# Kernel tuning notes

Measured on AMD Instinct MI355X. Metric: run time of the kernel, lower is better.

The kernel has to match this reference:

```python
import jax, jax.numpy as jnp
import numpy as np

N_NODES = 50000
N_EDGES = 1600000
IN_DIM, HID_DIM, OUT_DIM, HEADS = 128, 128, 64, 8
NEG_SLOPE = 0.2
BN_EPS = 1e-5


def setup_inputs() -> dict:
    key = jax.random.key(0)
    ks = jax.random.split(key, 12)
    hpc = HID_DIM // HEADS  # per-head channels of layer 1
    return {
        "x": jax.random.normal(ks[0], (N_NODES, IN_DIM), jnp.float32),
        "edge_index": jax.random.randint(ks[1], (2, N_EDGES), 0, N_NODES, jnp.int64),
        "W1": jax.random.normal(ks[2], (IN_DIM, HEADS * hpc), jnp.float32) * 0.05,
        "a1_src": jax.random.normal(ks[3], (HEADS, hpc), jnp.float32) * 0.1,
        "a1_dst": jax.random.normal(ks[4], (HEADS, hpc), jnp.float32) * 0.1,
        "b1": jnp.zeros((HEADS * hpc,), jnp.float32),
        "bn_gamma": jnp.ones((HID_DIM,), jnp.float32),
        "bn_beta": jnp.zeros((HID_DIM,), jnp.float32),
        "W2": jax.random.normal(ks[5], (HID_DIM, OUT_DIM), jnp.float32) * 0.05,
        "a2_src": jax.random.normal(ks[6], (1, OUT_DIM), jnp.float32) * 0.1,
        "a2_dst": jax.random.normal(ks[7], (1, OUT_DIM), jnp.float32) * 0.1,
        "b2": jnp.zeros((OUT_DIM,), jnp.float32),
    }


def _gat_conv(x, src, dst, W, a_src, a_dst, bias, heads, n_nodes):
    # x: [N, Fin]; src/dst: [E'] (self-loops already appended)
    hpc = W.shape[1] // heads
    h = (x @ W).reshape(n_nodes, heads, hpc)                 # [N,H,C]
    alpha_s = jnp.einsum("nhc,hc->nh", h, a_src)             # [N,H]
    alpha_d = jnp.einsum("nhc,hc->nh", h, a_dst)
    e = alpha_s[src] + alpha_d[dst]                          # [E',H]
    e = jax.nn.leaky_relu(e, NEG_SLOPE)
    # segment softmax over destination neighborhoods
    m = jax.ops.segment_max(e, dst, num_segments=n_nodes)    # [N,H]
    m = jnp.where(jnp.isfinite(m), m, 0.0)
    ee = jnp.exp(e - m[dst])
    denom = jax.ops.segment_sum(ee, dst, num_segments=n_nodes)
    alpha = ee / (denom[dst] + 1e-16)                        # [E',H]
    msg = h[src] * alpha[:, :, None]                         # [E',H,C]
    out = jax.ops.segment_sum(msg, dst, num_segments=n_nodes)  # [N,H,C]
    return out.reshape(n_nodes, heads * hpc) + bias


def _batch_norm(x, gamma, beta):
    mu = jnp.mean(x, axis=0)
    var = jnp.var(x, axis=0)
    return gamma * (x - mu) * jax.lax.rsqrt(var + BN_EPS) + beta


def reference(x, edge_index, W1, a1_src, a1_dst, b1, bn_gamma, bn_beta, W2, a2_src, a2_dst, b2):
    n = x.shape[0]
    loops = jnp.arange(n, dtype=edge_index.dtype)
    src = jnp.concatenate([edge_index[0], loops])            # PyG add_self_loops
    dst = jnp.concatenate([edge_index[1], loops])
    h = _gat_conv(x, src, dst, W1, a1_src, a1_dst, b1, HEADS, n)
    h = _batch_norm(h, bn_gamma, bn_beta)
    h = jax.nn.elu(h)
    # dropout: identity at inference
    out = _gat_conv(h, src, dst, W2, a2_src, a2_dst, b2, 1, n)
    return out
```

## Files before the change

kernel.cpp:

```cpp
#include <hip/hip_runtime.h>
#include <hip/hip_bf16.h>

#define N_NODES 50000
#define N_EDGES 1600000
#define HEADS 8
#define NBK 196
#define NBLK 196
#define EPB 8192

typedef unsigned short u16;
typedef unsigned char u8;
typedef unsigned int u32;
typedef __attribute__((ext_vector_type(8))) short bf16x8;
typedef __attribute__((ext_vector_type(4))) float f32x4;

__device__ __forceinline__ float bf2f(u16 u) {
  union { u32 i; float f; } v; v.i = ((u32)u) << 16; return v.f;
}
__device__ __forceinline__ float bflo(u32 p) {
  union { u32 i; float f; } v; v.i = p << 16; return v.f;
}
__device__ __forceinline__ float bfhi(u32 p) {
  union { u32 i; float f; } v; v.i = p & 0xffff0000u; return v.f;
}
__device__ __forceinline__ u16 f2bf(float f) {
  union { float f; u32 i; } v; v.f = f;
  u32 r = v.i + 0x7fff + ((v.i >> 16) & 1);
  return (u16)(r >> 16);
}
__device__ __forceinline__ u32 pack2(float a, float b) {
  return (u32)f2bf(a) | ((u32)f2bf(b) << 16);
}
__device__ __forceinline__ int rfl(int x) { return __builtin_amdgcn_readfirstlane(x); }

__global__ void k_detect(const u16* __restrict__ x, const u32* __restrict__ ei,
                         int* __restrict__ flags) {
  __shared__ int cbig, cnz;
  if (threadIdx.x == 0) { cbig = 0; cnz = 0; }
  __syncthreads();
  int lb = 0, ln = 0;
  for (int i = threadIdx.x; i < 4096; i += 256) {
    int ex = (x[i] >> 7) & 0xff;
    lb += (ex >= 140);
    if (i < 2048) ln += (ei[2 * i + 1] != 0);
  }
  atomicAdd(&cbig, lb); atomicAdd(&cnz, ln);
  __syncthreads();
  if (threadIdx.x == 0) {
    flags[0] = (cbig > 16) ? 1 : 0;
    flags[1] = (cnz == 0) ? 1 : 0;
  }
}

__global__ void k_convsmall(const void* a1s, const void* a1d, const void* b1,
                            const void* gam, const void* bet, const void* a2s,
                            const void* a2d, const void* b2, const void* W1,
                            const void* W2, float* __restrict__ smallf,
                            u16* __restrict__ w1t, u16* __restrict__ w2t,
                            const int* __restrict__ flags) {
  int i = blockIdx.x * 256 + threadIdx.x;
  if (i >= 25408) return;
  bool f32 = flags[0] != 0;
  auto ld = [&](const void* p, int off) -> float {
    return f32 ? ((const float*)p)[off] : bf2f(((const u16*)p)[off]);
  };
  if (i >= 17216) {
    int j = i - 17216, n = j >> 7, k = j & 127;
    w2t[j] = f2bf(ld(W2, k * 64 + n));
  } else if (i >= 832) {
    int j = i - 832, n = j >> 7, k = j & 127;
    w1t[j] = f2bf(ld(W1, k * 128 + n));
  } else {
    const void* src; int off;
    if (i >= 768)      { src = b2;  off = i - 768; }
    else if (i >= 704) { src = a2d; off = i - 704; }
    else if (i >= 640) { src = a2s; off = i - 640; }
    else if (i >= 512) { src = bet; off = i - 512; }
    else if (i >= 384) { src = gam; off = i - 384; }
    else if (i >= 256) { src = b1;  off = i - 256; }
    else if (i >= 128) { src = a1d; off = i - 128; }
    else               { src = a1s; off = i; }
    smallf[i] = ld(src, off);
  }
}

__global__ __launch_bounds__(256) void k_hist(const int* __restrict__ ei,
                                              int* __restrict__ H,
                                              int* __restrict__ totals,
                                              const int* __restrict__ flags) {
  __shared__ int hist[NBK];
  int t = threadIdx.x, blk = blockIdx.x;
  for (int i = t; i < NBK; i += 256) hist[i] = 0;
  __syncthreads();
  bool i64 = flags[1] != 0;
  int base = blk * EPB;
  for (int k = 0; k < 32; k++) {
    int e = base + k * 256 + t;
    if (e < N_EDGES) {
      int d = i64 ? ei[2 * (N_EDGES + e)] : ei[N_EDGES + e];
      atomicAdd(&hist[d >> 8], 1);
    }
  }
  __syncthreads();
  for (int i = t; i < NBK; i += 256) {
    H[i * NBLK + blk] = hist[i];
    atomicAdd(&totals[i], hist[i]);
  }
}

__global__ void k_scan_tot(const int* __restrict__ totals, int* __restrict__ bucketBase) {
  __shared__ int tmp[256];
  int t = threadIdx.x;
  int v = (t < NBK) ? totals[t] : 0;
  tmp[t] = v; __syncthreads();
  for (int o = 1; o < 256; o <<= 1) {
    int x = (t >= o) ? tmp[t - o] : 0; __syncthreads();
    tmp[t] += x; __syncthreads();
  }
  if (t < NBK) bucketBase[t] = tmp[t] - v;
  if (t == NBK - 1) bucketBase[NBK] = tmp[t];
}

__global__ void k_scan_blk(const int* __restrict__ H, const int* __restrict__ bucketBase,
                           int* __restrict__ P) {
  __shared__ int tmp[256];
  int t = threadIdx.x, b = blockIdx.x;
  int v = (t < NBLK) ? H[b * NBLK + t] : 0;
  tmp[t] = v; __syncthreads();
  for (int o = 1; o < 256; o <<= 1) {
    int x = (t >= o) ? tmp[t - o] : 0; __syncthreads();
    tmp[t] += x; __syncthreads();
  }
  if (t < NBLK) P[b * NBLK + t] = bucketBase[b] + tmp[t] - v;
}

__global__ __launch_bounds__(256) void k_bucket(const int* __restrict__ ei,
                                                const int* __restrict__ P,
                                                u32* __restrict__ buf,
                                                const int* __restrict__ flags) {
  __shared__ u32 sv[EPB];
  __shared__ u16 rank[EPB];
  __shared__ u8  sk8[EPB];
  __shared__ int cnt[NBK], scn[NBK], tmp[256];
  int t = threadIdx.x, blk = blockIdx.x;
  int base = blk * EPB;
  int nE = N_EDGES - base; if (nE > EPB) nE = EPB;
  for (int i = t; i < NBK; i += 256) cnt[i] = 0;
  __syncthreads();
  bool i64 = flags[1] != 0;
  for (int k = 0; k < EPB / 256; k++) {
    int li = k * 256 + t, e = base + li;
    if (li < nE) {
      int d = i64 ? ei[2 * (N_EDGES + e)] : ei[N_EDGES + e];
      rank[li] = (u16)atomicAdd(&cnt[d >> 8], 1);
    }
  }
  __syncthreads();
  int v = (t < NBK) ? cnt[t] : 0;
  tmp[t] = v; __syncthreads();
  for (int o = 1; o < 256; o <<= 1) {
    int x = (t >= o) ? tmp[t - o] : 0; __syncthreads();
    tmp[t] += x; __syncthreads();
  }
  if (t < NBK) scn[t] = tmp[t] - v;
  __syncthreads();
  for (int k = 0; k < EPB / 256; k++) {
    int li = k * 256 + t, e = base + li;
    if (li < nE) {
      int s = i64 ? ei[2 * e] : ei[e];
      int d = i64 ? ei[2 * (N_EDGES + e)] : ei[N_EDGES + e];
      int key = d >> 8;
      int pos = scn[key] + rank[li];
      sv[pos] = ((u32)(d & 255) << 16) | (u32)s;
      sk8[pos] = (u8)key;
    }
  }
  __syncthreads();
  for (int i = t; i < nE; i += 256) {
    int b = sk8[i];
    buf[P[b * NBLK + blk] + (i - scn[b])] = sv[i];
  }
}

__global__ __launch_bounds__(256) void k_csr(const u32* __restrict__ buf,
                                             const int* __restrict__ bucketBase,
                                             int* __restrict__ row_start,
                                             int* __restrict__ deg,
                                             int* __restrict__ csr, int N) {
  __shared__ int cnt[256], scn[256], cur[256];
  int b = blockIdx.x, t = threadIdx.x;
  int lo = bucketBase[b], hi = bucketBase[b + 1];
  cnt[t] = 0; __syncthreads();
  for (int e = lo + t; e < hi; e += 256) atomicAdd(&cnt[(buf[e] >> 16) & 255], 1);
  __syncthreads();
  int v = cnt[t];
  scn[t] = v; __syncthreads();
  for (int o = 1; o < 256; o <<= 1) {
    int x = (t >= o) ? scn[t - o] : 0; __syncthreads();
    scn[t] += x; __syncthreads();
  }
  int excl = scn[t] - v;
  int node = b * 256 + t;
  if (node < N) { row_start[node] = lo + excl; deg[node] = v; }
  cur[t] = lo + excl;
  __syncthreads();
  for (int e = lo + t; e < hi; e += 256) {
    u32 p = buf[e];
    int pos = atomicAdd(&cur[(p >> 16) & 255], 1);
    csr[pos] = p & 0xffff;
  }
}

template <int NCOLS, bool EPI, bool ALPHA1, bool AFLAG>
__global__ __launch_bounds__(256) void k_gemm_mfma(const void* __restrict__ A,
                                                   const u16* __restrict__ BT,
                                                   const float* __restrict__ scale,
                                                   const float* __restrict__ shift,
                                                   const float* __restrict__ va,
                                                   const float* __restrict__ vb,
                                                   float* __restrict__ as_out,
                                                   float* __restrict__ ad_out,
                                                   u16* __restrict__ C, int M,
                                                   const int* __restrict__ flags) {
  constexpr int KP = 136;
  constexpr int NT = NCOLS / 16;
  __shared__ u16 As[64 * KP];
  __shared__ u16 Bs[NCOLS * KP];
  int t = threadIdx.x;
  int row0 = blockIdx.x * 64;
  bool af32 = AFLAG ? (flags[0] != 0) : false;

  for (int i = t; i < NCOLS * 16; i += 256) {
    int n = i >> 4, q = i & 15;
    *(uint4*)&Bs[n * KP + q * 8] = ((const uint4*)BT)[n * 16 + q];
  }
  for (int i = t; i < 64 * 32; i += 256) {
    int r = i >> 5, c4 = i & 31;
    int row = row0 + r;
    uint2 pk = make_uint2(0u, 0u);
    if (row < M) {
      if (EPI) {
        uint2 p = ((const uint2*)A)[(size_t)row * 32 + c4];
        int c = c4 * 4;
        float v0 = bflo(p.x), v1 = bfhi(p.x), v2 = bflo(p.y), v3 = bfhi(p.y);
        v0 = fmaf(v0, scale[c],     shift[c]);     v0 = v0 > 0.f ? v0 : __expf(v0) - 1.f;
        v1 = fmaf(v1, scale[c + 1], shift[c + 1]); v1 = v1 > 0.f ? v1 : __expf(v1) - 1.f;
        v2 = fmaf(v2, scale[c + 2], shift[c + 2]); v2 = v2 > 0.f ? v2 : __expf(v2) - 1.f;
        v3 = fmaf(v3, scale[c + 3], shift[c + 3]); v3 = v3 > 0.f ? v3 : __expf(v3) - 1.f;
        pk.x = pack2(v0, v1); pk.y = pack2(v2, v3);
      } else if (af32) {
        float4 v = ((const float4*)A)[(size_t)row * 32 + c4];
        pk.x = pack2(v.x, v.y); pk.y = pack2(v.z, v.w);
      } else {
        pk = ((const uint2*)A)[(size_t)row * 32 + c4];
      }
    }
    *(uint2*)&As[r * KP + c4 * 4] = pk;
  }
  __syncthreads();

  int lane = t & 63, w = t >> 6;
  int m = lane & 15, quad = lane >> 4;
  f32x4 acc[NT];
#pragma unroll
  for (int nt = 0; nt < NT; nt++) acc[nt] = (f32x4)(0.f);
  const u16* aBase = &As[(w * 16 + m) * KP + quad * 8];
  const u16* bBase = &Bs[m * KP + quad * 8];
#pragma unroll
  for (int ks = 0; ks < 4; ks++) {
    bf16x8 af = *(const bf16x8*)(aBase + ks * 32);
#pragma unroll
    for (int nt = 0; nt < NT; nt++) {
      bf16x8 bf = *(const bf16x8*)(bBase + nt * 16 * KP + ks * 32);
      acc[nt] = __builtin_amdgcn_mfma_f32_16x16x32_bf16(af, bf, acc[nt], 0, 0, 0);
    }
  }
  int orow0 = row0 + w * 16 + quad * 4;
#pragma unroll
  for (int nt = 0; nt < NT; nt++) {
#pragma unroll
    for (int r = 0; r < 4; r++) {
      int row = orow0 + r;
      if (row < M) C[(size_t)row * NCOLS + nt * 16 + m] = f2bf(acc[nt][r]);
    }
  }
  if (ALPHA1) {
    float pav[NT], pbv[NT];
#pragma unroll
    for (int nt = 0; nt < NT; nt++) { pav[nt] = va[nt * 16 + m]; pbv[nt] = vb[nt * 16 + m]; }
#pragma unroll
    for (int r = 0; r < 4; r++) {
      int row = orow0 + r;
#pragma unroll
      for (int nt = 0; nt < NT; nt++) {
        float vs = acc[nt][r] * pav[nt];
        float vd = acc[nt][r] * pbv[nt];
        vs += __shfl_xor(vs, 1); vd += __shfl_xor(vd, 1);
        vs += __shfl_xor(vs, 2); vd += __shfl_xor(vd, 2);
        vs += __shfl_xor(vs, 4); vd += __shfl_xor(vd, 4);
        vs += __shfl_xor(vs, 8); vd += __shfl_xor(vd, 8);
        if (row < M && m == 0) { as_out[row * 8 + nt] = vs; ad_out[row * 8 + nt] = vd; }
      }
    }
  }
  if (EPI) {
    float pav[NT], pbv[NT];
#pragma unroll
    for (int nt = 0; nt < NT; nt++) { pav[nt] = va[nt * 16 + m]; pbv[nt] = vb[nt * 16 + m]; }
#pragma unroll
    for (int r = 0; r < 4; r++) {
      float vs = 0.f, vd = 0.f;
#pragma unroll
      for (int nt = 0; nt < NT; nt++) {
        vs = fmaf(acc[nt][r], pav[nt], vs);
        vd = fmaf(acc[nt][r], pbv[nt], vd);
      }
      vs += __shfl_xor(vs, 1); vd += __shfl_xor(vd, 1);
      vs += __shfl_xor(vs, 2); vd += __shfl_xor(vd, 2);
      vs += __shfl_xor(vs, 4); vd += __shfl_xor(vd, 4);
      vs += __shfl_xor(vs, 8); vd += __shfl_xor(vd, 8);
      int row = orow0 + r;
      if (row < M && m == 0) { as_out[row] = vs; ad_out[row] = vd; }
    }
  }
}

__global__ __launch_bounds__(256) void k_agg1(const u16* __restrict__ h1b,
                                              const float* __restrict__ as_,
                                              const float* __restrict__ ad_,
                                              const int* __restrict__ csr,
                                              const int* __restrict__ row_start,
                                              const int* __restrict__ deg,
                                              const float* __restrict__ b1,
                                              u16* __restrict__ out,
                                              float* __restrict__ bnrep, int N) {
  __shared__ float lsum[128], lsq[128];
  int t = threadIdx.x;
  if (t < 128) { lsum[t] = 0.f; lsq[t] = 0.f; }
  __syncthreads();
  int node = blockIdx.x * 4 + (t >> 6);
  int l = t & 63;
  int head = l >> 3, sub = l & 7;
  int eh = l >> 5, c2 = l & 31;
  int hch = c2 >> 2;
  if (node < N) {
    int node_u = rfl(node);
    int st = rfl(row_start[node_u]);
    int cnt = rfl(deg[node_u]);
    const int* cp = csr + st;
    const uint2* h2p = (const uint2*)h1b;
    float ad = ad_[(node_u << 3) | head];
    float sp = 0.f, a0 = 0.f, a1 = 0.f, a2 = 0.f, a3 = 0.f;
    int j = 0;
    for (; j + 8 <= cnt; j += 8) {
      int ssub = cp[j + sub];
      float e = as_[(ssub << 3) | head] + ad;
      e = fmaxf(e, 0.2f * e);
      float p = __expf(e);
      sp += p;
#pragma unroll
      for (int k = 0; k < 4; k++) {
        int se = cp[j + 2 * k], so = cp[j + 2 * k + 1];
        int sk = eh ? so : se;
        float pk = __shfl(p, (hch << 3) | (2 * k + eh));
        uint2 hv = h2p[(size_t)sk * 32 + c2];
        a0 = fmaf(pk, bflo(hv.x), a0); a1 = fmaf(pk, bfhi(hv.x), a1);
        a2 = fmaf(pk, bflo(hv.y), a2); a3 = fmaf(pk, bfhi(hv.y), a3);
      }
    }
    for (; j <= cnt; j++) {
      int s0 = (j < cnt) ? rfl(cp[j]) : node_u;
      float e = as_[(s0 << 3) | head] + ad;
      e = fmaxf(e, 0.2f * e);
      float p = __expf(e);
      if (sub == 0) sp += p;
      float pk = __shfl(p, hch << 3);
      if (eh == 0) {
        uint2 hv = h2p[(size_t)s0 * 32 + c2];
        a0 = fmaf(pk, bflo(hv.x), a0); a1 = fmaf(pk, bfhi(hv.x), a1);
        a2 = fmaf(pk, bflo(hv.y), a2); a3 = fmaf(pk, bfhi(hv.y), a3);
      }
    }
    sp += __shfl_xor(sp, 1);
    sp += __shfl_xor(sp, 2);
    sp += __shfl_xor(sp, 4);
    float inv = 1.f / (__shfl(sp, hch << 3) + 1e-16f);
    a0 += __shfl_xor(a0, 32); a1 += __shfl_xor(a1, 32);
    a2 += __shfl_xor(a2, 32); a3 += __shfl_xor(a3, 32);
    if (eh == 0) {
      int c0 = c2 * 4;
      float r0 = fmaf(a0, inv, b1[c0]);
      float r1 = fmaf(a1, inv, b1[c0 + 1]);
      float r2 = fmaf(a2, inv, b1[c0 + 2]);
      float r3 = fmaf(a3, inv, b1[c0 + 3]);
      ((uint2*)out)[(size_t)node_u * 32 + c2] = make_uint2(pack2(r0, r1), pack2(r2, r3));
      atomicAdd(&lsum[c0], r0);     atomicAdd(&lsq[c0], r0 * r0);
      atomicAdd(&lsum[c0 + 1], r1); atomicAdd(&lsq[c0 + 1], r1 * r1);
      atomicAdd(&lsum[c0 + 2], r2); atomicAdd(&lsq[c0 + 2], r2 * r2);
      atomicAdd(&lsum[c0 + 3], r3); atomicAdd(&lsq[c0 + 3], r3 * r3);
    }
  }
  __syncthreads();
  if (t < 128) {
    int rep = (blockIdx.x & 31) * 256;
    atomicAdd(&bnrep[rep + t], lsum[t]);
    atomicAdd(&bnrep[rep + 128 + t], lsq[t]);
  }
}

__global__ void k_bnfin(const float* __restrict__ bnrep,
                        const float* __restrict__ gamma, const float* __restrict__ beta,
                        float* __restrict__ scale, float* __restrict__ shift, int N) {
  int t = threadIdx.x;
  if (t >= 128) return;
  float s = 0.f, q = 0.f;
  for (int r = 0; r < 32; r++) {
    s += bnrep[r * 256 + t];
    q += bnrep[r * 256 + 128 + t];
  }
  float mu = s / (float)N;
  float var = fmaxf(q / (float)N - mu * mu, 0.f);
  float sc = gamma[t] * rsqrtf(var + 1e-5f);
  scale[t] = sc;
  shift[t] = beta[t] - mu * sc;
}

__global__ __launch_bounds__(256) void k_agg2(const u16* __restrict__ h2b,
                                              const float* __restrict__ as_,
                                              const float* __restrict__ ad_,
                                              const int* __restrict__ csr,
                                              const int* __restrict__ row_start,
                                              const int* __restrict__ deg,
                                              const float* __restrict__ b2,
                                              void* __restrict__ out,
                                              const int* __restrict__ flags, int N) {
  int node = blockIdx.x * 4 + (threadIdx.x >> 6);
  if (node >= N) return;
  int l = threadIdx.x & 63;
  int sub = l & 7;
  int e4 = l >> 4, c4 = l & 15;
  int node_u = rfl(node);
  int st = rfl(row_start[node_u]);
  int cnt = rfl(deg[node_u]);
  const int* cp = csr + st;
  const uint2* h2p = (const uint2*)h2b;
  float ad = ad_[node_u];
  float sp = 0.f, a0 = 0.f, a1 = 0.f, a2 = 0.f, a3 = 0.f;
  int j = 0;
  for (; j + 8 <= cnt; j += 8) {
    int ssub = cp[j + sub];
    float e = as_[ssub] + ad;
    e = fmaxf(e, 0.2f * e);
    float p = __expf(e);
    if (l < 8) sp += p;
#pragma unroll
    for (int pass = 0; pass < 2; pass++) {
      int sa = cp[j + 4 * pass], sb = cp[j + 4 * pass + 1];
      int sc = cp[j + 4 * pass + 2], sd = cp[j + 4 * pass + 3];
      int sk = (e4 == 0) ? sa : (e4 == 1) ? sb : (e4 == 2) ? sc : sd;
      float pk = __shfl(p, 4 * pass + e4);
      uint2 hv = h2p[(size_t)sk * 16 + c4];
      a0 = fmaf(pk, bflo(hv.x), a0); a1 = fmaf(pk, bfhi(hv.x), a1);
      a2 = fmaf(pk, bflo(hv.y), a2); a3 = fmaf(pk, bfhi(hv.y), a3);
    }
  }
  for (; j <= cnt; j++) {
    int s0 = (j < cnt) ? rfl(cp[j]) : node_u;
    float e = as_[s0] + ad;
    e = fmaxf(e, 0.2f * e);
    float p = __expf(e);
    if (l == 0) sp += p;
    float pk = __shfl(p, 0);
    if (e4 == 0) {
      uint2 hv = h2p[(size_t)s0 * 16 + c4];
      a0 = fmaf(pk, bflo(hv.x), a0); a1 = fmaf(pk, bfhi(hv.x), a1);
      a2 = fmaf(pk, bflo(hv.y), a2); a3 = fmaf(pk, bfhi(hv.y), a3);
    }
  }
  sp += __shfl_xor(sp, 1);
  sp += __shfl_xor(sp, 2);
  sp += __shfl_xor(sp, 4);
  float inv = 1.f / (__shfl(sp, 0) + 1e-16f);
  a0 += __shfl_xor(a0, 16); a1 += __shfl_xor(a1, 16);
  a2 += __shfl_xor(a2, 16); a3 += __shfl_xor(a3, 16);
  a0 += __shfl_xor(a0, 32); a1 += __shfl_xor(a1, 32);
  a2 += __shfl_xor(a2, 32); a3 += __shfl_xor(a3, 32);
  if (e4 == 0) {
    int c0 = c4 * 4;
    float r0 = fmaf(a0, inv, b2[c0]);
    float r1 = fmaf(a1, inv, b2[c0 + 1]);
    float r2 = fmaf(a2, inv, b2[c0 + 2]);
    float r3 = fmaf(a3, inv, b2[c0 + 3]);
    if (flags[0]) {
      ((float4*)out)[(size_t)node_u * 16 + c4] = make_float4(r0, r1, r2, r3);
    } else {
      ((uint2*)out)[(size_t)node_u * 16 + c4] = make_uint2(pack2(r0, r1), pack2(r2, r3));
    }
  }
}

extern "C" void kernel_launch(void* const* d_in, const int* in_sizes, int n_in,
                              void* d_out, int out_size, void* d_ws, size_t ws_size,
                              hipStream_t stream) {
  const void* x   = d_in[0];
  const int*  ei  = (const int*)d_in[1];
  const void* W1  = d_in[2];
  const void* a1s = d_in[3];
  const void* a1d = d_in[4];
  const void* b1  = d_in[5];
  const void* gam = d_in[6];
  const void* bet = d_in[7];
  const void* W2  = d_in[8];
  const void* a2s = d_in[9];
  const void* a2d = d_in[10];
  const void* b2  = d_in[11];

  char* ws = (char*)d_ws;
  size_t off = 0;
  auto alloc = [&](size_t bytes) -> void* {
    void* p = ws + off;
    off += (bytes + 255) & ~(size_t)255;
    return p;
  };
  int* flags = (int*)alloc(256);
  char* zreg = (char*)alloc(1024 + 32 * 256 * 4);
  int* totals = (int*)zreg;
  float* bnrep = (float*)(zreg + 1024);
  int* H  = (int*)alloc((size_t)NBK * NBLK * 4);
  int* P  = (int*)alloc((size_t)NBK * NBLK * 4);
  int* bucketBase = (int*)alloc(1024);
  u32* ebuf = (u32*)alloc((size_t)N_EDGES * 4);
  int* csr = (int*)alloc((size_t)N_EDGES * 4);
  int* row_start = (int*)alloc((size_t)N_NODES * 4);
  int* deg = (int*)alloc((size_t)N_NODES * 4);
  float* smallf = (float*)alloc(832 * 4);
  float* a1sf = smallf;        float* a1df = smallf + 128;
  float* b1f  = smallf + 256;  float* gamf = smallf + 384;
  float* betf = smallf + 512;  float* a2sf = smallf + 640;
  float* a2df = smallf + 704;  float* b2f  = smallf + 768;
  u16* w1t = (u16*)alloc(16384 * 2);
  u16* w2t = (u16*)alloc(8192 * 2);
  u16* h1b  = (u16*)alloc((size_t)N_NODES * 128 * 2);
  u16* h1ob = (u16*)alloc((size_t)N_NODES * 128 * 2);
  u16* h2b  = (u16*)alloc((size_t)N_NODES * 64 * 2);
  float* al1s = (float*)alloc((size_t)N_NODES * 8 * 4);
  float* al1d = (float*)alloc((size_t)N_NODES * 8 * 4);
  float* scale = (float*)alloc(512);
  float* shift = (float*)alloc(512);
  float* al2s = (float*)alloc((size_t)N_NODES * 4);
  float* al2d = (float*)alloc((size_t)N_NODES * 4);
  if (off > ws_size) return;

  hipMemsetAsync(zreg, 0, 1024 + 32 * 256 * 4, stream);
  k_detect<<<1, 256, 0, stream>>>((const u16*)x, (const u32*)ei, flags);
  k_convsmall<<<100, 256, 0, stream>>>(a1s, a1d, b1, gam, bet, a2s, a2d, b2, W1, W2,
                                       smallf, w1t, w2t, flags);

  k_hist<<<NBLK, 256, 0, stream>>>(ei, H, totals, flags);
  k_scan_tot<<<1, 256, 0, stream>>>(totals, bucketBase);
  k_scan_blk<<<NBK, 256, 0, stream>>>(H, bucketBase, P);
  k_bucket<<<NBLK, 256, 0, stream>>>(ei, P, ebuf, flags);
  k_csr<<<NBK, 256, 0, stream>>>(ebuf, bucketBase, row_start, deg, csr, N_NODES);

  k_gemm_mfma<128, false, true, true><<<(N_NODES + 63) / 64, 256, 0, stream>>>(
      x, w1t, nullptr, nullptr, a1sf, a1df, al1s, al1d, h1b, N_NODES, flags);
  k_agg1<<<(N_NODES + 3) / 4, 256, 0, stream>>>(h1b, al1s, al1d, csr, row_start, deg,
                                                b1f, h1ob, bnrep, N_NODES);
  k_bnfin<<<1, 128, 0, stream>>>(bnrep, gamf, betf, scale, shift, N_NODES);

  k_gemm_mfma<64, true, false, false><<<(N_NODES + 63) / 64, 256, 0, stream>>>(
      h1ob, w2t, scale, shift, a2sf, a2df, al2s, al2d, h2b, N_NODES, flags);
  k_agg2<<<(N_NODES + 3) / 4, 256, 0, stream>>>(h2b, al2s, al2d, csr, row_start, deg,
                                                b2f, d_out, flags, N_NODES);
}
```

Baseline: 370.0 us.

## Fold scan and BN-finalize kernels into consumers; move BN stats to separate pass

```diff
diff --git a/kernel.cpp b/kernel.cpp
--- a/kernel.cpp
+++ b/kernel.cpp
@@ -108,30 +108,24 @@
   }
 }
 
-__global__ void k_scan_tot(const int* __restrict__ totals, int* __restrict__ bucketBase) {
-  __shared__ int tmp[256];
-  int t = threadIdx.x;
-  int v = (t < NBK) ? totals[t] : 0;
-  tmp[t] = v; __syncthreads();
+__global__ void k_scan_blk(const int* __restrict__ H, const int* __restrict__ totals,
+                           int* __restrict__ P) {
+  __shared__ int tb[256], tmp[256];
+  int t = threadIdx.x, b = blockIdx.x;
+  int v0 = (t < NBK) ? totals[t] : 0;
+  tb[t] = v0; __syncthreads();
   for (int o = 1; o < 256; o <<= 1) {
-    int x = (t >= o) ? tmp[t - o] : 0; __syncthreads();
-    tmp[t] += x; __syncthreads();
-  }
-  if (t < NBK) bucketBase[t] = tmp[t] - v;
-  if (t == NBK - 1) bucketBase[NBK] = tmp[t];
-}
-
-__global__ void k_scan_blk(const int* __restrict__ H, const int* __restrict__ bucketBase,
-                           int* __restrict__ P) {
-  __shared__ int tmp[256];
-  int t = threadIdx.x, b = blockIdx.x;
+    int x = (t >= o) ? tb[t - o] : 0; __syncthreads();
+    tb[t] += x; __syncthreads();
+  }
+  int base = (b == 0) ? 0 : tb[b - 1];
   int v = (t < NBLK) ? H[b * NBLK + t] : 0;
   tmp[t] = v; __syncthreads();
   for (int o = 1; o < 256; o <<= 1) {
     int x = (t >= o) ? tmp[t - o] : 0; __syncthreads();
     tmp[t] += x; __syncthreads();
   }
-  if (t < NBLK) P[b * NBLK + t] = bucketBase[b] + tmp[t] - v;
+  if (t < NBLK) P[b * NBLK + t] = base + tmp[t] - v;
 }
 
 __global__ __launch_bounds__(256) void k_bucket(const int* __restrict__ ei,
@@ -183,13 +177,20 @@
 }
 
 __global__ __launch_bounds__(256) void k_csr(const u32* __restrict__ buf,
-                                             const int* __restrict__ bucketBase,
+                                             const int* __restrict__ totals,
                                              int* __restrict__ row_start,
                                              int* __restrict__ deg,
                                              int* __restrict__ csr, int N) {
-  __shared__ int cnt[256], scn[256], cur[256];
+  __shared__ int tb[256], cnt[256], scn[256], cur[256];
   int b = blockIdx.x, t = threadIdx.x;
-  int lo = bucketBase[b], hi = bucketBase[b + 1];
+  int v0 = (t < NBK) ? totals[t] : 0;
+  tb[t] = v0; __syncthreads();
+  for (int o = 1; o < 256; o <<= 1) {
+    int x = (t >= o) ? tb[t - o] : 0; __syncthreads();
+    tb[t] += x; __syncthreads();
+  }
+  int lo = (b == 0) ? 0 : tb[b - 1];
+  int hi = tb[b];
   cnt[t] = 0; __syncthreads();
   for (int e = lo + t; e < hi; e += 256) atomicAdd(&cnt[(buf[e] >> 16) & 255], 1);
   __syncthreads();
@@ -214,8 +215,10 @@
 template <int NCOLS, bool EPI, bool ALPHA1, bool AFLAG>
 __global__ __launch_bounds__(256) void k_gemm_mfma(const void* __restrict__ A,
                                                    const u16* __restrict__ BT,
-                                                   const float* __restrict__ scale,
-                                                   const float* __restrict__ shift,
+                                                   const float* __restrict__ bnsum,
+                                                   const float* __restrict__ bnsq,
+                                                   const float* __restrict__ gamma,
+                                                   const float* __restrict__ beta,
                                                    const float* __restrict__ va,
                                                    const float* __restrict__ vb,
                                                    float* __restrict__ as_out,
@@ -226,9 +229,20 @@
   constexpr int NT = NCOLS / 16;
   __shared__ u16 As[64 * KP];
   __shared__ u16 Bs[NCOLS * KP];
+  __shared__ float sSc[128], sSh[128];
   int t = threadIdx.x;
   int row0 = blockIdx.x * 64;
   bool af32 = AFLAG ? (flags[0] != 0) : false;
+
+  if (EPI) {
+    if (t < 128) {
+      float mu = bnsum[t] * (1.f / (float)N_NODES);
+      float var = fmaxf(bnsq[t] * (1.f / (float)N_NODES) - mu * mu, 0.f);
+      float sc = gamma[t] * rsqrtf(var + 1e-5f);
+      sSc[t] = sc; sSh[t] = beta[t] - mu * sc;
+    }
+    __syncthreads();
+  }
 
   for (int i = t; i < NCOLS * 16; i += 256) {
     int n = i >> 4, q = i & 15;
@@ -243,10 +257,10 @@
         uint2 p = ((const uint2*)A)[(size_t)row * 32 + c4];
         int c = c4 * 4;
         float v0 = bflo(p.x), v1 = bfhi(p.x), v2 = bflo(p.y), v3 = bfhi(p.y);
-        v0 = fmaf(v0, scale[c],     shift[c]);     v0 = v0 > 0.f ? v0 : __expf(v0) - 1.f;
-        v1 = fmaf(v1, scale[c + 1], shift[c + 1]); v1 = v1 > 0.f ? v1 : __expf(v1) - 1.f;
-        v2 = fmaf(v2, scale[c + 2], shift[c + 2]); v2 = v2 > 0.f ? v2 : __expf(v2) - 1.f;
-        v3 = fmaf(v3, scale[c + 3], shift[c + 3]); v3 = v3 > 0.f ? v3 : __expf(v3) - 1.f;
+        v0 = fmaf(v0, sSc[c],     sSh[c]);     v0 = v0 > 0.f ? v0 : __expf(v0) - 1.f;
+        v1 = fmaf(v1, sSc[c + 1], sSh[c + 1]); v1 = v1 > 0.f ? v1 : __expf(v1) - 1.f;
+        v2 = fmaf(v2, sSc[c + 2], sSh[c + 2]); v2 = v2 > 0.f ? v2 : __expf(v2) - 1.f;
+        v3 = fmaf(v3, sSc[c + 3], sSh[c + 3]); v3 = v3 > 0.f ? v3 : __expf(v3) - 1.f;
         pk.x = pack2(v0, v1); pk.y = pack2(v2, v3);
       } else if (af32) {
         float4 v = ((const float4*)A)[(size_t)row * 32 + c4];
@@ -332,97 +346,84 @@
                                               const int* __restrict__ row_start,
                                               const int* __restrict__ deg,
                                               const float* __restrict__ b1,
-                                              u16* __restrict__ out,
-                                              float* __restrict__ bnrep, int N) {
-  __shared__ float lsum[128], lsq[128];
-  int t = threadIdx.x;
-  if (t < 128) { lsum[t] = 0.f; lsq[t] = 0.f; }
-  __syncthreads();
-  int node = blockIdx.x * 4 + (t >> 6);
-  int l = t & 63;
+                                              u16* __restrict__ out, int N) {
+  int node = blockIdx.x * 4 + (threadIdx.x >> 6);
+  if (node >= N) return;
+  int l = threadIdx.x & 63;
   int head = l >> 3, sub = l & 7;
   int eh = l >> 5, c2 = l & 31;
   int hch = c2 >> 2;
-  if (node < N) {
-    int node_u = rfl(node);
-    int st = rfl(row_start[node_u]);
-    int cnt = rfl(deg[node_u]);
-    const int* cp = csr + st;
-    const uint2* h2p = (const uint2*)h1b;
-    float ad = ad_[(node_u << 3) | head];
-    float sp = 0.f, a0 = 0.f, a1 = 0.f, a2 = 0.f, a3 = 0.f;
-    int j = 0;
-    for (; j + 8 <= cnt; j += 8) {
-      int ssub = cp[j + sub];
-      float e = as_[(ssub << 3) | head] + ad;
-      e = fmaxf(e, 0.2f * e);
-      float p = __expf(e);
-      sp += p;
-#pragma unroll
-      for (int k = 0; k < 4; k++) {
-        int se = cp[j + 2 * k], so = cp[j + 2 * k + 1];
-        int sk = eh ? so : se;
-        float pk = __shfl(p, (hch << 3) | (2 * k + eh));
-        uint2 hv = h2p[(size_t)sk * 32 + c2];
-        a0 = fmaf(pk, bflo(hv.x), a0); a1 = fmaf(pk, bfhi(hv.x), a1);
-        a2 = fmaf(pk, bflo(hv.y), a2); a3 = fmaf(pk, bfhi(hv.y), a3);
-      }
-    }
-    for (; j <= cnt; j++) {
-      int s0 = (j < cnt) ? rfl(cp[j]) : node_u;
-      float e = as_[(s0 << 3) | head] + ad;
-      e = fmaxf(e, 0.2f * e);
-      float p = __expf(e);
-      if (sub == 0) sp += p;
-      float pk = __shfl(p, hch << 3);
-      if (eh == 0) {
-        uint2 hv = h2p[(size_t)s0 * 32 + c2];
-        a0 = fmaf(pk, bflo(hv.x), a0); a1 = fmaf(pk, bfhi(hv.x), a1);
-        a2 = fmaf(pk, bflo(hv.y), a2); a3 = fmaf(pk, bfhi(hv.y), a3);
-      }
-    }
-    sp += __shfl_xor(sp, 1);
-    sp += __shfl_xor(sp, 2);
-    sp += __shfl_xor(sp, 4);
-    float inv = 1.f / (__shfl(sp, hch << 3) + 1e-16f);
-    a0 += __shfl_xor(a0, 32); a1 += __shfl_xor(a1, 32);
-    a2 += __shfl_xor(a2, 32); a3 += __shfl_xor(a3, 32);
+  int node_u = rfl(node);
+  int st = rfl(row_start[node_u]);
+  int cnt = rfl(deg[node_u]);
+  const int* cp = csr + st;
+  const uint2* h2p = (const uint2*)h1b;
+  float ad = ad_[(node_u << 3) | head];
+  float sp = 0.f, a0 = 0.f, a1 = 0.f, a2 = 0.f, a3 = 0.f;
+  int j = 0;
+  for (; j + 8 <= cnt; j += 8) {
+    int ssub = cp[j + sub];
+    float e = as_[(ssub << 3) | head] + ad;
+    e = fmaxf(e, 0.2f * e);
+    float p = __expf(e);
+    sp += p;
+#pragma unroll
+    for (int k = 0; k < 4; k++) {
+      int se = cp[j + 2 * k], so = cp[j + 2 * k + 1];
+      int sk = eh ? so : se;
+      float pk = __shfl(p, (hch << 3) | (2 * k + eh));
+      uint2 hv = h2p[(size_t)sk * 32 + c2];
+      a0 = fmaf(pk, bflo(hv.x), a0); a1 = fmaf(pk, bfhi(hv.x), a1);
+      a2 = fmaf(pk, bflo(hv.y), a2); a3 = fmaf(pk, bfhi(hv.y), a3);
+    }
+  }
+  for (; j <= cnt; j++) {
+    int s0 = (j < cnt) ? rfl(cp[j]) : node_u;
+    float e = as_[(s0 << 3) | head] + ad;
+    e = fmaxf(e, 0.2f * e);
+    float p = __expf(e);
+    if (sub == 0) sp += p;
+    float pk = __shfl(p, hch << 3);
     if (eh == 0) {
-      int c0 = c2 * 4;
-      float r0 = fmaf(a0, inv, b1[c0]);
-      float r1 = fmaf(a1, inv, b1[c0 + 1]);
-      float r2 = fmaf(a2, inv, b1[c0 + 2]);
-      float r3 = fmaf(a3, inv, b1[c0 + 3]);
-      ((uint2*)out)[(size_t)node_u * 32 + c2] = make_uint2(pack2(r0, r1), pack2(r2, r3));
-      atomicAdd(&lsum[c0], r0);     atomicAdd(&lsq[c0], r0 * r0);
-      atomicAdd(&lsum[c0 + 1], r1); atomicAdd(&lsq[c0 + 1], r1 * r1);
-      atomicAdd(&lsum[c0 + 2], r2); atomicAdd(&lsq[c0 + 2], r2 * r2);
-      atomicAdd(&lsum[c0 + 3], r3); atomicAdd(&lsq[c0 + 3], r3 * r3);
-    }
-  }
-  __syncthreads();
+      uint2 hv = h2p[(size_t)s0 * 32 + c2];
+      a0 = fmaf(pk, bflo(hv.x), a0); a1 = fmaf(pk, bfhi(hv.x), a1);
+      a2 = fmaf(pk, bflo(hv.y), a2); a3 = fmaf(pk, bfhi(hv.y), a3);
+    }
+  }
+  sp += __shfl_xor(sp, 1);
+  sp += __shfl_xor(sp, 2);
+  sp += __shfl_xor(sp, 4);
+  float inv = 1.f / (__shfl(sp, hch << 3) + 1e-16f);
+  a0 += __shfl_xor(a0, 32); a1 += __shfl_xor(a1, 32);
+  a2 += __shfl_xor(a2, 32); a3 += __shfl_xor(a3, 32);
+  if (eh == 0) {
+    int c0 = c2 * 4;
+    float r0 = fmaf(a0, inv, b1[c0]);
+    float r1 = fmaf(a1, inv, b1[c0 + 1]);
+    float r2 = fmaf(a2, inv, b1[c0 + 2]);
+    float r3 = fmaf(a3, inv, b1[c0 + 3]);
+    ((uint2*)out)[(size_t)node_u * 32 + c2] = make_uint2(pack2(r0, r1), pack2(r2, r3));
+  }
+}
+
+__global__ void k_bnstat(const u16* __restrict__ h, float* __restrict__ gsum,
+                         float* __restrict__ gsq, int N) {
+  __shared__ float ts[256], tq[256];
+  int t = threadIdx.x, col = t & 127, rr = t >> 7;
+  int row0 = blockIdx.x * 128;
+  float s = 0.f, q = 0.f;
+  for (int r = rr; r < 128; r += 2) {
+    int row = row0 + r;
+    if (row < N) {
+      float v = bf2f(h[((size_t)row << 7) + col]);
+      s += v; q = fmaf(v, v, q);
+    }
+  }
+  ts[t] = s; tq[t] = q; __syncthreads();
   if (t < 128) {
-    int rep = (blockIdx.x & 31) * 256;
-    atomicAdd(&bnrep[rep + t], lsum[t]);
-    atomicAdd(&bnrep[rep + 128 + t], lsq[t]);
-  }
-}
-
-__global__ void k_bnfin(const float* __restrict__ bnrep,
-                        const float* __restrict__ gamma, const float* __restrict__ beta,
-                        float* __restrict__ scale, float* __restrict__ shift, int N) {
-  int t = threadIdx.x;
-  if (t >= 128) return;
-  float s = 0.f, q = 0.f;
-  for (int r = 0; r < 32; r++) {
-    s += bnrep[r * 256 + t];
-    q += bnrep[r * 256 + 128 + t];
-  }
-  float mu = s / (float)N;
-  float var = fmaxf(q / (float)N - mu * mu, 0.f);
-  float sc = gamma[t] * rsqrtf(var + 1e-5f);
-  scale[t] = sc;
-  shift[t] = beta[t] - mu * sc;
+    atomicAdd(&gsum[t], ts[t] + ts[t + 128]);
+    atomicAdd(&gsq[t], tq[t] + tq[t + 128]);
+  }
 }
 
 __global__ __launch_bounds__(256) void k_agg2(const u16* __restrict__ h2b,
@@ -523,12 +524,12 @@
     return p;
   };
   int* flags = (int*)alloc(256);
-  char* zreg = (char*)alloc(1024 + 32 * 256 * 4);
+  char* zreg = (char*)alloc(2048);
   int* totals = (int*)zreg;
-  float* bnrep = (float*)(zreg + 1024);
+  float* gsum = (float*)(zreg + 1024);
+  float* gsq  = gsum + 128;
   int* H  = (int*)alloc((size_t)NBK * NBLK * 4);
   int* P  = (int*)alloc((size_t)NBK * NBLK * 4);
-  int* bucketBase = (int*)alloc(1024);
   u32* ebuf = (u32*)alloc((size_t)N_EDGES * 4);
   int* csr = (int*)alloc((size_t)N_EDGES * 4);
   int* row_start = (int*)alloc((size_t)N_NODES * 4);
@@ -545,31 +546,30 @@
   u16* h2b  = (u16*)alloc((size_t)N_NODES * 64 * 2);
   float* al1s = (float*)alloc((size_t)N_NODES * 8 * 4);
   float* al1d = (float*)alloc((size_t)N_NODES * 8 * 4);
-  float* scale = (float*)alloc(512);
-  float* shift = (float*)alloc(512);
   float* al2s = (float*)alloc((size_t)N_NODES * 4);
   float* al2d = (float*)alloc((size_t)N_NODES * 4);
   if (off > ws_size) return;
 
-  hipMemsetAsync(zreg, 0, 1024 + 32 * 256 * 4, stream);
+  hipMemsetAsync(zreg, 0, 2048, stream);
   k_detect<<<1, 256, 0, stream>>>((const u16*)x, (const u32*)ei, flags);
   k_convsmall<<<100, 256, 0, stream>>>(a1s, a1d, b1, gam, bet, a2s, a2d, b2, W1, W2,
                                        smallf, w1t, w2t, flags);
 
   k_hist<<<NBLK, 256, 0, stream>>>(ei, H, totals, flags);
-  k_scan_tot<<<1, 256, 0, stream>>>(totals, bucketBase);
-  k_scan_blk<<<NBK, 256, 0, stream>>>(H, bucketBase, P);
+  k_scan_blk<<<NBK, 256, 0, stream>>>(H, totals, P);
   k_bucket<<<NBLK, 256, 0, stream>>>(ei, P, ebuf, flags);
-  k_csr<<<NBK, 256, 0, stream>>>(ebuf, bucketBase, row_start, deg, csr, N_NODES);
+  k_csr<<<NBK, 256, 0, stream>>>(ebuf, totals, row_start, deg, csr, N_NODES);
 
   k_gemm_mfma<128, false, true, true><<<(N_NODES + 63) / 64, 256, 0, stream>>>(
-      x, w1t, nullptr, nullptr, a1sf, a1df, al1s, al1d, h1b, N_NODES, flags);
+      x, w1t, nullptr, nullptr, nullptr, nullptr, a1sf, a1df, al1s, al1d,
+      h1b, N_NODES, flags);
   k_agg1<<<(N_NODES + 3) / 4, 256, 0, stream>>>(h1b, al1s, al1d, csr, row_start, deg,
-                                                b1f, h1ob, bnrep, N_NODES);
-  k_bnfin<<<1, 128, 0, stream>>>(bnrep, gamf, betf, scale, shift, N_NODES);
+                                                b1f, h1ob, N_NODES);
+  k_bnstat<<<(N_NODES + 127) / 128, 256, 0, stream>>>(h1ob, gsum, gsq, N_NODES);
 
   k_gemm_mfma<64, true, false, false><<<(N_NODES + 63) / 64, 256, 0, stream>>>(
-      h1ob, w2t, scale, shift, a2sf, a2df, al2s, al2d, h2b, N_NODES, flags);
+      h1ob, w2t, gsum, gsq, gamf, betf, a2sf, a2df, al2s, al2d,
+      h2b, N_NODES, flags);
   k_agg2<<<(N_NODES + 3) / 4, 256, 0, stream>>>(h2b, al2s, al2d, csr, row_start, deg,
                                                 b2f, d_out, flags, N_NODES);
 }
```

Measured after the change: 357.7 us. -3.3%, faster.
